# Optimization experiments

Measured on AMD Instinct MI355X. Metric: run time of the kernel, lower is better.

Reference implementation:

```python
import jax, jax.numpy as jnp
import numpy as np

VOCAB = 50000
D = 128      # word_embedding_size
H = 64       # attention_hidden_dim


def _doc_embed(words, emb_table, w_self, b_self):
    """words: (..., W) int -> (..., D) via tanh self-attention pooling over words."""
    we = emb_table[words]                                # (..., W, D)
    scores = jnp.tanh(we @ w_self + b_self)              # (..., W, 1)
    wgt = jax.nn.softmax(scores, axis=-2)                # softmax over word dim
    return jnp.sum(wgt * we, axis=-2)                    # (..., D)


def _attention(reviews_emb, query_emb, Wq, bq, w_red):
    """reviews_emb: (B,R,D), query_emb: (B,1,D) -> (B,D)."""
    B = query_emb.shape[0]
    pq = jnp.tanh(query_emb.reshape(B, D) @ Wq + bq)     # (B, D*H)
    pq = pq.reshape(B, D, H)
    s = jnp.einsum('brd,bdh->brh', reviews_emb, pq)      # (B,R,H)
    r = s @ w_red                                        # (B,R,1)
    w = jax.nn.softmax(r, axis=1)                        # softmax over reviews
    return jnp.sum(w * reviews_emb, axis=1)              # (B,D)


def setup_inputs() -> dict:
    key = jax.random.key(0)
    ks = jax.random.split(key, 9)
    B, R, W = 256, 20, 100
    user = jax.random.randint(ks[0], (B, R, W), 0, VOCAB)
    item = jax.random.randint(ks[1], (B, R, W), 0, VOCAB)
    query = jax.random.randint(ks[2], (B, W), 0, VOCAB)
    emb_table = jax.random.normal(ks[3], (VOCAB, D), dtype=jnp.float32) * 0.01
    w_self = jax.random.normal(ks[4], (D, 1), dtype=jnp.float32) * (1.0 / np.sqrt(D))
    b_self = jax.random.uniform(ks[5], (1,), dtype=jnp.float32, maxval=0.01)
    Wq = jax.random.normal(ks[6], (D, D * H), dtype=jnp.float32) * (1.0 / np.sqrt(D))
    bq = jax.random.uniform(ks[7], (D * H,), dtype=jnp.float32, maxval=0.01)
    w_red = jax.random.normal(ks[8], (H, 1), dtype=jnp.float32) * (1.0 / np.sqrt(H))
    pf = jnp.float32(0.5)  # personalized_factor
    return {"user_reviews_words": user, "item_reviews_words": item, "query": query,
            "emb_table": emb_table, "w_self": w_self, "b_self": b_self,
            "Wq": Wq, "bq": bq, "w_red": w_red, "pf": pf}


def reference(user_reviews_words, item_reviews_words, query,
              emb_table, w_self, b_self, Wq, bq, w_red, pf):
    # mode == 'test'
    user_emb = _doc_embed(user_reviews_words, emb_table, w_self, b_self)   # (B,R,D)
    item_emb = _doc_embed(item_reviews_words, emb_table, w_self, b_self)   # (B,R,D)
    q_emb = _doc_embed(query[:, None, :], emb_table, w_self, b_self)       # (B,1,D)
    user_entity = _attention(user_emb, q_emb, Wq, bq, w_red)               # (B,D)
    item_entity = _attention(item_emb, q_emb, Wq, bq, w_red)               # (B,D)
    personalized = user_entity + pf * q_emb[:, 0, :]
    return (personalized, item_entity)
```

## Files before the change

### kernel.cpp

```cpp
#include <hip/hip_runtime.h>
#include <math.h>

#define D 128
#define H 64
#define W 100
#define R 20
#define NB 256
#define NDOC_UI (NB * R)
#define NDOC    (2 * NDOC_UI + NB)
#define VOCAB 50000

__device__ __forceinline__ float fast_tanh(float x) {
    float u = __expf(2.0f * x);
    return 1.0f - 2.0f * __builtin_amdgcn_rcpf(1.0f + u);
}
__device__ __forceinline__ float fast_exp_tanh(float x) {
    return __expf(fast_tanh(x));
}

__device__ __forceinline__ unsigned short f2bf(float f) {
    unsigned int b = __float_as_uint(f);
    b += 0x7fffu + ((b >> 16) & 1u);
    return (unsigned short)(b >> 16);
}

__global__ __launch_bounds__(256) void vocab_prep_kernel(
    const float* __restrict__ emb, const float* __restrict__ w_self,
    const float* __restrict__ b_self,
    ushort* __restrict__ emb_bf, float* __restrict__ evocab)
{
    int tid = threadIdx.x, lane32 = tid & 31, grp = tid >> 5;
    int row = blockIdx.x * 8 + grp;
    float4 v   = ((const float4*)emb)[row * 32 + lane32];
    float4 ws4 = ((const float4*)w_self)[lane32];
    float p = v.x * ws4.x + v.y * ws4.y + v.z * ws4.z + v.w * ws4.w;
    p += __shfl_xor(p, 16, 64);
    p += __shfl_xor(p, 8, 64);
    p += __shfl_xor(p, 4, 64);
    p += __shfl_xor(p, 2, 64);
    p += __shfl_xor(p, 1, 64);
    float e = __expf(tanhf(p + b_self[0]));
    if (lane32 == 0) evocab[row] = e;
    ushort4 u;
    u.x = f2bf(v.x * e); u.y = f2bf(v.y * e);
    u.z = f2bf(v.z * e); u.w = f2bf(v.w * e);
    int q = lane32 >> 3;
    ushort4* dst = (ushort4*)(emb_bf + (size_t)q * VOCAB * 32);
    dst[row * 8 + (lane32 & 7)] = u;
}

__global__ __launch_bounds__(128) void doc_embed_bf16_kernel(
    const int* __restrict__ user_w, const int* __restrict__ item_w,
    const int* __restrict__ query_w,
    const ushort* __restrict__ emb_bf, const float* __restrict__ evocab,
    float* __restrict__ user_emb, float* __restrict__ item_emb,
    float* __restrict__ q_emb)
{
    int tid    = threadIdx.x;
    int lane32 = tid & 31;
    int grp    = tid >> 5;
    unsigned B    = blockIdx.x;
    unsigned quar = (B & 7) >> 1;
    unsigned sub  = (B >> 3) * 2 + (B & 1);
    int doc = (int)sub * 4 + grp;

    const int* wp; float* outp;
    if (doc < NDOC_UI)        { wp = user_w + doc * W;               outp = user_emb + doc * D; }
    else if (doc < 2*NDOC_UI) { int t = doc - NDOC_UI;   wp = item_w  + t * W; outp = item_emb + t * D; }
    else                      { int t = doc - 2*NDOC_UI; wp = query_w + t * W; outp = q_emb    + t * D; }

    int wreg[4];
    #pragma unroll
    for (int k = 0; k < 4; ++k) {
        int idx = k * 32 + lane32;
        wreg[k] = wp[idx > W - 1 ? W - 1 : idx];
    }

    float ep = 0.f;
    #pragma unroll
    for (int k = 0; k < 4; ++k) {
        float e = evocab[wreg[k]];
        if (k < 3 || lane32 < 4) ep += e;
    }
    ep += __shfl_xor(ep, 16, 64);
    ep += __shfl_xor(ep, 8, 64);
    ep += __shfl_xor(ep, 4, 64);
    ep += __shfl_xor(ep, 2, 64);
    ep += __shfl_xor(ep, 1, 64);
    float inv = 1.f / ep;

    int permbase = (tid & 32) << 2;
    int wsub     = lane32 >> 2;
    int sext     = lane32 & 3;

    float acc[8];
    #pragma unroll
    for (int j = 0; j < 8; ++j) acc[j] = 0.f;

    const uint4* eq4 = (const uint4*)(emb_bf + (size_t)quar * VOCAB * 32);

    #pragma unroll
    for (int c = 0; c < 2; ++c) {
        const int n  = (c == 0) ? 7 : 6;
        const int s0 = (c == 0) ? 0 : 7;
        int wid[7]; uint4 v[7];
        for (int j = 0; j < n; ++j) {
            int s = s0 + j;
            wid[j] = __builtin_amdgcn_ds_bpermute(
                permbase | ((((8 * s) & 31) + wsub) << 2), wreg[s >> 2]);
        }
        for (int j = 0; j < n; ++j)
            v[j] = eq4[(size_t)(unsigned)wid[j] * 4 + sext];
        for (int j = 0; j < n; ++j) {
            if (s0 + j == 12 && wsub >= 4) break;
            uint4 x = v[j];
            acc[0] += __uint_as_float(x.x << 16);
            acc[1] += __uint_as_float(x.x & 0xffff0000u);
            acc[2] += __uint_as_float(x.y << 16);
            acc[3] += __uint_as_float(x.y & 0xffff0000u);
            acc[4] += __uint_as_float(x.z << 16);
            acc[5] += __uint_as_float(x.z & 0xffff0000u);
            acc[6] += __uint_as_float(x.w << 16);
            acc[7] += __uint_as_float(x.w & 0xffff0000u);
        }
    }

    #pragma unroll
    for (int j = 0; j < 8; ++j) {
        acc[j] += __shfl_xor(acc[j], 4, 64);
        acc[j] += __shfl_xor(acc[j], 8, 64);
        acc[j] += __shfl_xor(acc[j], 16, 64);
    }

    if (wsub == 0) {
        float* o = outp + quar * 32 + sext * 8;
        *(float4*)o       = make_float4(acc[0]*inv, acc[1]*inv, acc[2]*inv, acc[3]*inv);
        *(float4*)(o + 4) = make_float4(acc[4]*inv, acc[5]*inv, acc[6]*inv, acc[7]*inv);
    }
}

__global__ __launch_bounds__(256, 7) void doc_embed_fp32_kernel(
    const int* __restrict__ user_w, const int* __restrict__ item_w,
    const int* __restrict__ query_w,
    const float* __restrict__ emb, const float* __restrict__ w_self,
    const float* __restrict__ b_self,
    float* __restrict__ user_emb, float* __restrict__ item_emb,
    float* __restrict__ q_emb)
{
    int tid    = threadIdx.x;
    int lane32 = tid & 31;
    int grp    = tid >> 5;
    int doc    = blockIdx.x * 8 + grp;

    const int* wp; float* outp;
    if (doc < NDOC_UI)        { wp = user_w + doc * W;               outp = user_emb + doc * D; }
    else if (doc < 2*NDOC_UI) { int t = doc - NDOC_UI;   wp = item_w  + t * W; outp = item_emb + t * D; }
    else                      { int t = doc - 2*NDOC_UI; wp = query_w + t * W; outp = q_emb    + t * D; }

    int wreg[4];
    #pragma unroll
    for (int k = 0; k < 4; ++k) {
        int idx = k * 32 + lane32;
        wreg[k] = wp[idx > W - 1 ? W - 1 : idx];
    }

    float4 ws4 = ((const float4*)w_self)[lane32];
    float  bs  = b_self[0];
    const float4* emb4 = (const float4*)emb;
    int permbase = (tid & 32) * 4;

    float4 acc  = make_float4(0.f, 0.f, 0.f, 0.f);
    float  esum = 0.f;

    #pragma unroll
    for (int c = 0; c < 10; ++c) {
        int word[10];
        #pragma unroll
        for (int j = 0; j < 10; ++j) {
            int w = c * 10 + j;
            word[j] = __builtin_amdgcn_ds_bpermute(permbase | ((w & 31) * 4),
                                                   wreg[w >> 5]);
        }
        float4 v[10];
        #pragma unroll
        for (int j = 0; j < 10; ++j)
            v[j] = emb4[(size_t)word[j] * 32 + lane32];

        #pragma unroll
        for (int j = 0; j < 10; ++j) {
            float p = v[j].x * ws4.x + v[j].y * ws4.y + v[j].z * ws4.z + v[j].w * ws4.w;
            p += __shfl_xor(p, 16, 64);
            p += __shfl_xor(p, 8, 64);
            p += __shfl_xor(p, 4, 64);
            p += __shfl_xor(p, 2, 64);
            p += __shfl_xor(p, 1, 64);
            float e = fast_exp_tanh(p + bs);
            esum += e;
            acc.x += e * v[j].x;
            acc.y += e * v[j].y;
            acc.z += e * v[j].z;
            acc.w += e * v[j].w;
        }
    }

    float inv = 1.0f / esum;
    acc.x *= inv; acc.y *= inv; acc.z *= inv; acc.w *= inv;
    ((float4*)outp)[lane32] = acc;
}

__global__ __launch_bounds__(256) void pv_kernel(
    const float* __restrict__ q_emb, const float* __restrict__ Wq,
    const float* __restrict__ bq, const float* __restrict__ w_red,
    float* __restrict__ pv)
{
    __shared__ __align__(16) float Wb[128 * 68];

    int dd  = blockIdx.x;
    int m0g = blockIdx.y * 128;
    int tid = threadIdx.x;

    {
        int rrow = tid >> 4;
        int f4   = tid & 15;
        #pragma unroll
        for (int pass = 0; pass < 8; ++pass) {
            int k = pass * 16 + rrow;
            float4 vw = ((const float4*)Wq)[k * 2048 + dd * 16 + f4];
            *(float4*)&Wb[k * 68 + f4 * 4] = vw;
        }
    }
    __syncthreads();

    int nthr = tid & 15;
    int mthr = tid >> 4;
    int n0 = nthr * 4;
    const float4* q4 = (const float4*)q_emb;
    int mbase = (m0g + mthr * 8) * 32;

    float acc[8][4];
    #pragma unroll
    for (int i = 0; i < 8; ++i)
        #pragma unroll
        for (int j = 0; j < 4; ++j) acc[i][j] = 0.f;

    float4 qa[8], qb[8];
    #pragma unroll
    for (int i = 0; i < 8; ++i) qa[i] = q4[mbase + i * 32];

    for (int k4 = 0; k4 < 32; ++k4) {
        if (k4 < 31) {
            #pragma unroll
            for (int i = 0; i < 8; ++i) qb[i] = q4[mbase + i * 32 + k4 + 1];
        }
        #pragma unroll
        for (int kk = 0; kk < 4; ++kk) {
            float4 wv = *(const float4*)&Wb[(k4 * 4 + kk) * 68 + n0];
            #pragma unroll
            for (int i = 0; i < 8; ++i) {
                float a = (kk == 0) ? qa[i].x : (kk == 1) ? qa[i].y
                        : (kk == 2) ? qa[i].z : qa[i].w;
                acc[i][0] += a * wv.x;
                acc[i][1] += a * wv.y;
                acc[i][2] += a * wv.z;
                acc[i][3] += a * wv.w;
            }
        }
        #pragma unroll
        for (int i = 0; i < 8; ++i) qa[i] = qb[i];
    }

    float4 bqv = ((const float4*)bq)[dd * 16 + nthr];
    float4 wrv = ((const float4*)w_red)[nthr];

    #pragma unroll
    for (int i = 0; i < 8; ++i) {
        float s = fast_tanh(acc[i][0] + bqv.x) * wrv.x
                + fast_tanh(acc[i][1] + bqv.y) * wrv.y
                + fast_tanh(acc[i][2] + bqv.z) * wrv.z
                + fast_tanh(acc[i][3] + bqv.w) * wrv.w;
        s += __shfl_xor(s, 1, 64);
        s += __shfl_xor(s, 2, 64);
        s += __shfl_xor(s, 4, 64);
        s += __shfl_xor(s, 8, 64);
        if (nthr == 0) pv[(m0g + mthr * 8 + i) * 128 + dd] = s;
    }
}

__global__ __launch_bounds__(256) void attn_kernel(
    const float* __restrict__ user_emb, const float* __restrict__ item_emb,
    const float* __restrict__ q_emb, const float* __restrict__ pv,
    const float* __restrict__ pf, float* __restrict__ out)
{
    __shared__ float rev[R * 129];
    __shared__ float pvl[D];
    __shared__ float sc[R];

    int b   = blockIdx.x;
    int set = blockIdx.y;
    const float* revg = (set == 0 ? user_emb : item_emb) + b * R * D;
    int tid = threadIdx.x;

    for (int idx = tid; idx < R * D; idx += 256)
        rev[(idx >> 7) * 129 + (idx & 127)] = revg[idx];
    if (tid < D) pvl[tid] = pv[b * D + tid];
    __syncthreads();

    if (tid < R) {
        float s = 0.f;
        const float* row = &rev[tid * 129];
        #pragma unroll 16
        for (int k = 0; k < D; ++k) s += row[k] * pvl[k];
        sc[tid] = s;
    }
    __syncthreads();

    float m = -1e30f;
    for (int r = 0; r < R; ++r) m = fmaxf(m, sc[r]);
    float sum = 0.f;
    for (int r = 0; r < R; ++r) sum += __expf(sc[r] - m);
    float inv = 1.f / sum;

    if (tid < D) {
        float acc = 0.f;
        for (int r = 0; r < R; ++r)
            acc += __expf(sc[r] - m) * inv * rev[r * 129 + tid];
        if (set == 0) {
            acc += pf[0] * q_emb[b * D + tid];
            out[b * D + tid] = acc;
        } else {
            out[NB * D + b * D + tid] = acc;
        }
    }
}

extern "C" void kernel_launch(void* const* d_in, const int* in_sizes, int n_in,
                              void* d_out, int out_size, void* d_ws, size_t ws_size,
                              hipStream_t stream) {
    const int*   user_w  = (const int*)d_in[0];
    const int*   item_w  = (const int*)d_in[1];
    const int*   query_w = (const int*)d_in[2];
    const float* emb     = (const float*)d_in[3];
    const float* w_self  = (const float*)d_in[4];
    const float* b_self  = (const float*)d_in[5];
    const float* Wq      = (const float*)d_in[6];
    const float* bq      = (const float*)d_in[7];
    const float* w_red   = (const float*)d_in[8];
    const float* pf      = (const float*)d_in[9];

    float* ws       = (float*)d_ws;
    float* user_emb = ws;
    float* item_emb = user_emb + NDOC_UI * D;
    float* q_emb    = item_emb + NDOC_UI * D;
    float* pv       = q_emb    + NB * D;
    float* evocab   = pv       + NB * D;
    ushort* emb_bf  = (ushort*)(evocab + VOCAB);
    float* out      = (float*)d_out;

    const size_t need_fast =
        (size_t)(2 * NDOC_UI * D + 2 * NB * D + VOCAB) * sizeof(float)
        + (size_t)VOCAB * D * sizeof(ushort);

    if (ws_size >= need_fast) {
        vocab_prep_kernel<<<VOCAB / 8, 256, 0, stream>>>(
            emb, w_self, b_self, emb_bf, evocab);
        doc_embed_bf16_kernel<<<NDOC, 128, 0, stream>>>(
            user_w, item_w, query_w, emb_bf, evocab, user_emb, item_emb, q_emb);
    } else {
        doc_embed_fp32_kernel<<<NDOC / 8, 256, 0, stream>>>(
            user_w, item_w, query_w, emb, w_self, b_self, user_emb, item_emb, q_emb);
    }
    pv_kernel<<<dim3(128, 2), 256, 0, stream>>>(q_emb, Wq, bq, w_red, pv);
    attn_kernel<<<dim3(NB, 2), 256, 0, stream>>>(user_emb, item_emb, q_emb, pv, pf, out);
}
```

Baseline: 146.3 us.

## Fuse all four stages into one persistent kernel with grid barriers

Replaces the vocab-prep, bf16 doc-embed, pv and attention launches with a single persistent kernel of 256 blocks of 512 threads. The stages are separated by atomic-counter grid barriers, and the counters are reset with a memset before each launch. This removes launch gaps and tail effects between kernels. In exchange, the doc-embed phase runs with only 256 resident blocks instead of thousands, which may lower memory-level parallelism for the gather. Correctness also depends on every block being co-resident.

```diff
diff --git a/kernel.cpp b/kernel.cpp
--- a/kernel.cpp
+++ b/kernel.cpp
@@ -9,6 +9,8 @@
 #define NDOC_UI (NB * R)
 #define NDOC    (2 * NDOC_UI + NB)
 #define VOCAB 50000
+#define GRID 256
+#define TPB  512
 
 __device__ __forceinline__ float fast_tanh(float x) {
     float u = __expf(2.0f * x);
@@ -24,118 +26,254 @@
     return (unsigned short)(b >> 16);
 }
 
-__global__ __launch_bounds__(256) void vocab_prep_kernel(
+__device__ __forceinline__ void grid_barrier(unsigned* cnt) {
+    __syncthreads();
+    if (threadIdx.x == 0) {
+        __hip_atomic_fetch_add(cnt, 1u, __ATOMIC_ACQ_REL, __HIP_MEMORY_SCOPE_AGENT);
+        while (__hip_atomic_load(cnt, __ATOMIC_ACQUIRE, __HIP_MEMORY_SCOPE_AGENT) < GRID)
+            __builtin_amdgcn_s_sleep(8);
+    }
+    __syncthreads();
+}
+
+__global__ __launch_bounds__(TPB, 4) void fused_kernel(
+    const int* __restrict__ user_w, const int* __restrict__ item_w,
+    const int* __restrict__ query_w,
     const float* __restrict__ emb, const float* __restrict__ w_self,
     const float* __restrict__ b_self,
-    ushort* __restrict__ emb_bf, float* __restrict__ evocab)
+    const float* __restrict__ Wq, const float* __restrict__ bq,
+    const float* __restrict__ w_red, const float* __restrict__ pf,
+    float* __restrict__ user_emb, float* __restrict__ item_emb,
+    float* __restrict__ q_emb, float* __restrict__ pv,
+    float* __restrict__ evocab, ushort* __restrict__ emb_bf,
+    unsigned* __restrict__ sync_cnt,
+    float* __restrict__ out)
 {
-    int tid = threadIdx.x, lane32 = tid & 31, grp = tid >> 5;
-    int row = blockIdx.x * 8 + grp;
-    float4 v   = ((const float4*)emb)[row * 32 + lane32];
-    float4 ws4 = ((const float4*)w_self)[lane32];
-    float p = v.x * ws4.x + v.y * ws4.y + v.z * ws4.z + v.w * ws4.w;
-    p += __shfl_xor(p, 16, 64);
-    p += __shfl_xor(p, 8, 64);
-    p += __shfl_xor(p, 4, 64);
-    p += __shfl_xor(p, 2, 64);
-    p += __shfl_xor(p, 1, 64);
-    float e = __expf(tanhf(p + b_self[0]));
-    if (lane32 == 0) evocab[row] = e;
-    ushort4 u;
-    u.x = f2bf(v.x * e); u.y = f2bf(v.y * e);
-    u.z = f2bf(v.z * e); u.w = f2bf(v.w * e);
-    int q = lane32 >> 3;
-    ushort4* dst = (ushort4*)(emb_bf + (size_t)q * VOCAB * 32);
-    dst[row * 8 + (lane32 & 7)] = u;
-}
-
-__global__ __launch_bounds__(128) void doc_embed_bf16_kernel(
-    const int* __restrict__ user_w, const int* __restrict__ item_w,
-    const int* __restrict__ query_w,
-    const ushort* __restrict__ emb_bf, const float* __restrict__ evocab,
-    float* __restrict__ user_emb, float* __restrict__ item_emb,
-    float* __restrict__ q_emb)
-{
-    int tid    = threadIdx.x;
-    int lane32 = tid & 31;
-    int grp    = tid >> 5;
-    unsigned B    = blockIdx.x;
-    unsigned quar = (B & 7) >> 1;
-    unsigned sub  = (B >> 3) * 2 + (B & 1);
-    int doc = (int)sub * 4 + grp;
-
-    const int* wp; float* outp;
-    if (doc < NDOC_UI)        { wp = user_w + doc * W;               outp = user_emb + doc * D; }
-    else if (doc < 2*NDOC_UI) { int t = doc - NDOC_UI;   wp = item_w  + t * W; outp = item_emb + t * D; }
-    else                      { int t = doc - 2*NDOC_UI; wp = query_w + t * W; outp = q_emb    + t * D; }
-
-    int wreg[4];
-    #pragma unroll
-    for (int k = 0; k < 4; ++k) {
-        int idx = k * 32 + lane32;
-        wreg[k] = wp[idx > W - 1 ? W - 1 : idx];
-    }
-
-    float ep = 0.f;
-    #pragma unroll
-    for (int k = 0; k < 4; ++k) {
-        float e = evocab[wreg[k]];
-        if (k < 3 || lane32 < 4) ep += e;
-    }
-    ep += __shfl_xor(ep, 16, 64);
-    ep += __shfl_xor(ep, 8, 64);
-    ep += __shfl_xor(ep, 4, 64);
-    ep += __shfl_xor(ep, 2, 64);
-    ep += __shfl_xor(ep, 1, 64);
-    float inv = 1.f / ep;
-
-    int permbase = (tid & 32) << 2;
-    int wsub     = lane32 >> 2;
-    int sext     = lane32 & 3;
-
-    float acc[8];
-    #pragma unroll
-    for (int j = 0; j < 8; ++j) acc[j] = 0.f;
-
-    const uint4* eq4 = (const uint4*)(emb_bf + (size_t)quar * VOCAB * 32);
-
-    #pragma unroll
-    for (int c = 0; c < 2; ++c) {
-        const int n  = (c == 0) ? 7 : 6;
-        const int s0 = (c == 0) ? 0 : 7;
-        int wid[7]; uint4 v[7];
-        for (int j = 0; j < n; ++j) {
-            int s = s0 + j;
-            wid[j] = __builtin_amdgcn_ds_bpermute(
-                permbase | ((((8 * s) & 31) + wsub) << 2), wreg[s >> 2]);
-        }
-        for (int j = 0; j < n; ++j)
-            v[j] = eq4[(size_t)(unsigned)wid[j] * 4 + sext];
-        for (int j = 0; j < n; ++j) {
-            if (s0 + j == 12 && wsub >= 4) break;
-            uint4 x = v[j];
-            acc[0] += __uint_as_float(x.x << 16);
-            acc[1] += __uint_as_float(x.x & 0xffff0000u);
-            acc[2] += __uint_as_float(x.y << 16);
-            acc[3] += __uint_as_float(x.y & 0xffff0000u);
-            acc[4] += __uint_as_float(x.z << 16);
-            acc[5] += __uint_as_float(x.z & 0xffff0000u);
-            acc[6] += __uint_as_float(x.w << 16);
-            acc[7] += __uint_as_float(x.w & 0xffff0000u);
-        }
-    }
-
-    #pragma unroll
-    for (int j = 0; j < 8; ++j) {
-        acc[j] += __shfl_xor(acc[j], 4, 64);
-        acc[j] += __shfl_xor(acc[j], 8, 64);
-        acc[j] += __shfl_xor(acc[j], 16, 64);
-    }
-
-    if (wsub == 0) {
-        float* o = outp + quar * 32 + sext * 8;
-        *(float4*)o       = make_float4(acc[0]*inv, acc[1]*inv, acc[2]*inv, acc[3]*inv);
-        *(float4*)(o + 4) = make_float4(acc[4]*inv, acc[5]*inv, acc[6]*inv, acc[7]*inv);
+    __shared__ __align__(16) float smem[128 * 68];
+    const int tid    = threadIdx.x;
+    const int bx     = blockIdx.x;
+    const int lane32 = tid & 31;
+
+    {
+        const int grp16 = tid >> 5;
+        float4 ws4 = ((const float4*)w_self)[lane32];
+        float  bs  = b_self[0];
+        for (int row = bx * 16 + grp16; row < VOCAB; row += GRID * 16) {
+            float4 v = ((const float4*)emb)[row * 32 + lane32];
+            float p = v.x * ws4.x + v.y * ws4.y + v.z * ws4.z + v.w * ws4.w;
+            p += __shfl_xor(p, 16, 64);
+            p += __shfl_xor(p, 8, 64);
+            p += __shfl_xor(p, 4, 64);
+            p += __shfl_xor(p, 2, 64);
+            p += __shfl_xor(p, 1, 64);
+            float e = __expf(tanhf(p + bs));
+            if (lane32 == 0) evocab[row] = e;
+            ushort4 u;
+            u.x = f2bf(v.x * e); u.y = f2bf(v.y * e);
+            u.z = f2bf(v.z * e); u.w = f2bf(v.w * e);
+            int q = lane32 >> 3;
+            ushort4* dst = (ushort4*)(emb_bf + (size_t)q * VOCAB * 32);
+            dst[row * 8 + (lane32 & 7)] = u;
+        }
+    }
+    grid_barrier(&sync_cnt[0]);
+
+    {
+        const int quar = (bx & 7) >> 1;
+        const int rb   = ((bx >> 3) << 1) | (bx & 1);
+        const int g    = tid >> 5;
+        const int permbase = (tid & 32) << 2;
+        const int wsub = lane32 >> 2;
+        const int sext = lane32 & 3;
+        const uint4* eq4 = (const uint4*)(emb_bf + (size_t)quar * VOCAB * 32);
+
+        for (int it = 0; it < 11; ++it) {
+            int local = it * 16 + g;
+            if (local >= 164) break;
+            int doc = rb * 164 + local;
+
+            const int* wp; float* outp;
+            if (doc < NDOC_UI)        { wp = user_w + doc * W;               outp = user_emb + doc * D; }
+            else if (doc < 2*NDOC_UI) { int t2 = doc - NDOC_UI;   wp = item_w  + t2 * W; outp = item_emb + t2 * D; }
+            else                      { int t2 = doc - 2*NDOC_UI; wp = query_w + t2 * W; outp = q_emb    + t2 * D; }
+
+            int wreg[4];
+            #pragma unroll
+            for (int k = 0; k < 4; ++k) {
+                int idx = k * 32 + lane32;
+                wreg[k] = wp[idx > W - 1 ? W - 1 : idx];
+            }
+
+            float ep = 0.f;
+            #pragma unroll
+            for (int k = 0; k < 4; ++k) {
+                float e = evocab[wreg[k]];
+                if (k < 3 || lane32 < 4) ep += e;
+            }
+            ep += __shfl_xor(ep, 16, 64);
+            ep += __shfl_xor(ep, 8, 64);
+            ep += __shfl_xor(ep, 4, 64);
+            ep += __shfl_xor(ep, 2, 64);
+            ep += __shfl_xor(ep, 1, 64);
+            float inv = 1.f / ep;
+
+            float acc[8];
+            #pragma unroll
+            for (int j = 0; j < 8; ++j) acc[j] = 0.f;
+
+            #pragma unroll
+            for (int c = 0; c < 2; ++c) {
+                const int n  = (c == 0) ? 7 : 6;
+                const int s0 = (c == 0) ? 0 : 7;
+                int wid[7]; uint4 v[7];
+                for (int j = 0; j < n; ++j) {
+                    int s = s0 + j;
+                    wid[j] = __builtin_amdgcn_ds_bpermute(
+                        permbase | ((((8 * s) & 31) + wsub) << 2), wreg[s >> 2]);
+                }
+                for (int j = 0; j < n; ++j)
+                    v[j] = eq4[(size_t)(unsigned)wid[j] * 4 + sext];
+                for (int j = 0; j < n; ++j) {
+                    if (s0 + j == 12 && wsub >= 4) break;
+                    uint4 x = v[j];
+                    acc[0] += __uint_as_float(x.x << 16);
+                    acc[1] += __uint_as_float(x.x & 0xffff0000u);
+                    acc[2] += __uint_as_float(x.y << 16);
+                    acc[3] += __uint_as_float(x.y & 0xffff0000u);
+                    acc[4] += __uint_as_float(x.z << 16);
+                    acc[5] += __uint_as_float(x.z & 0xffff0000u);
+                    acc[6] += __uint_as_float(x.w << 16);
+                    acc[7] += __uint_as_float(x.w & 0xffff0000u);
+                }
+            }
+
+            #pragma unroll
+            for (int j = 0; j < 8; ++j) {
+                acc[j] += __shfl_xor(acc[j], 4, 64);
+                acc[j] += __shfl_xor(acc[j], 8, 64);
+                acc[j] += __shfl_xor(acc[j], 16, 64);
+            }
+
+            if (wsub == 0) {
+                float* o = outp + quar * 32 + sext * 8;
+                *(float4*)o       = make_float4(acc[0]*inv, acc[1]*inv, acc[2]*inv, acc[3]*inv);
+                *(float4*)(o + 4) = make_float4(acc[4]*inv, acc[5]*inv, acc[6]*inv, acc[7]*inv);
+            }
+        }
+    }
+    grid_barrier(&sync_cnt[1]);
+
+    {
+        const int dd  = bx >> 1;
+        const int m0g = (bx & 1) * 128;
+        {
+            int rrow = tid >> 4;
+            int f4   = tid & 15;
+            #pragma unroll
+            for (int pass = 0; pass < 4; ++pass) {
+                int k = pass * 32 + rrow;
+                float4 vw = ((const float4*)Wq)[k * 2048 + dd * 16 + f4];
+                *(float4*)&smem[k * 68 + f4 * 4] = vw;
+            }
+        }
+        __syncthreads();
+
+        int nthr = tid & 15;
+        int mthr = tid >> 4;
+        int n0 = nthr * 4;
+        const float4* q4 = (const float4*)q_emb;
+        int mbase = m0g + mthr * 4;
+
+        float acc[4][4];
+        #pragma unroll
+        for (int i = 0; i < 4; ++i)
+            #pragma unroll
+            for (int j = 0; j < 4; ++j) acc[i][j] = 0.f;
+
+        float4 qa[4], qb[4];
+        #pragma unroll
+        for (int i = 0; i < 4; ++i) qa[i] = q4[(mbase + i) * 32];
+
+        for (int k4 = 0; k4 < 32; ++k4) {
+            if (k4 < 31) {
+                #pragma unroll
+                for (int i = 0; i < 4; ++i) qb[i] = q4[(mbase + i) * 32 + k4 + 1];
+            }
+            #pragma unroll
+            for (int kk = 0; kk < 4; ++kk) {
+                float4 wv = *(const float4*)&smem[(k4 * 4 + kk) * 68 + n0];
+                #pragma unroll
+                for (int i = 0; i < 4; ++i) {
+                    float a = (kk == 0) ? qa[i].x : (kk == 1) ? qa[i].y
+                            : (kk == 2) ? qa[i].z : qa[i].w;
+                    acc[i][0] += a * wv.x;
+                    acc[i][1] += a * wv.y;
+                    acc[i][2] += a * wv.z;
+                    acc[i][3] += a * wv.w;
+                }
+            }
+            #pragma unroll
+            for (int i = 0; i < 4; ++i) qa[i] = qb[i];
+        }
+
+        float4 bqv = ((const float4*)bq)[dd * 16 + nthr];
+        float4 wrv = ((const float4*)w_red)[nthr];
+
+        #pragma unroll
+        for (int i = 0; i < 4; ++i) {
+            float s = fast_tanh(acc[i][0] + bqv.x) * wrv.x
+                    + fast_tanh(acc[i][1] + bqv.y) * wrv.y
+                    + fast_tanh(acc[i][2] + bqv.z) * wrv.z
+                    + fast_tanh(acc[i][3] + bqv.w) * wrv.w;
+            s += __shfl_xor(s, 1, 64);
+            s += __shfl_xor(s, 2, 64);
+            s += __shfl_xor(s, 4, 64);
+            s += __shfl_xor(s, 8, 64);
+            if (nthr == 0) pv[(mbase + i) * 128 + dd] = s;
+        }
+    }
+    grid_barrier(&sync_cnt[2]);
+
+    {
+        const int b   = bx;
+        const int set = tid >> 8;
+        const int t   = tid & 255;
+        const float* revg = (set == 0 ? user_emb : item_emb) + b * R * D;
+        float* srev = smem + set * (R * 129);
+        float* pvl  = smem + 2 * (R * 129);
+        float* ssc  = smem + 2 * (R * 129) + D + set * 32;
+
+        for (int idx = t; idx < R * D; idx += 256)
+            srev[(idx >> 7) * 129 + (idx & 127)] = revg[idx];
+        if (tid < D) pvl[tid] = pv[b * D + tid];
+        __syncthreads();
+
+        if (t < R) {
+            float s = 0.f;
+            const float* row = &srev[t * 129];
+            #pragma unroll 16
+            for (int k = 0; k < D; ++k) s += row[k] * pvl[k];
+            ssc[t] = s;
+        }
+        __syncthreads();
+
+        float m = -1e30f;
+        for (int r = 0; r < R; ++r) m = fmaxf(m, ssc[r]);
+        float sum = 0.f;
+        for (int r = 0; r < R; ++r) sum += __expf(ssc[r] - m);
+        float inv = 1.f / sum;
+
+        if (t < D) {
+            float acc2 = 0.f;
+            for (int r = 0; r < R; ++r)
+                acc2 += __expf(ssc[r] - m) * inv * srev[r * 129 + t];
+            if (set == 0) {
+                acc2 += pf[0] * q_emb[b * D + t];
+                out[b * D + t] = acc2;
+            } else {
+                out[NB * D + b * D + t] = acc2;
+            }
+        }
     }
 }
 
@@ -354,21 +492,23 @@
     float* pv       = q_emb    + NB * D;
     float* evocab   = pv       + NB * D;
     ushort* emb_bf  = (ushort*)(evocab + VOCAB);
+    unsigned* sync_cnt = (unsigned*)(emb_bf + (size_t)VOCAB * D);
     float* out      = (float*)d_out;
 
     const size_t need_fast =
         (size_t)(2 * NDOC_UI * D + 2 * NB * D + VOCAB) * sizeof(float)
-        + (size_t)VOCAB * D * sizeof(ushort);
+        + (size_t)VOCAB * D * sizeof(ushort)
+        + 3 * sizeof(unsigned);
 
     if (ws_size >= need_fast) {
-        vocab_prep_kernel<<<VOCAB / 8, 256, 0, stream>>>(
-            emb, w_self, b_self, emb_bf, evocab);
-        doc_embed_bf16_kernel<<<NDOC, 128, 0, stream>>>(
-            user_w, item_w, query_w, emb_bf, evocab, user_emb, item_emb, q_emb);
+        hipMemsetAsync(sync_cnt, 0, 3 * sizeof(unsigned), stream);
+        fused_kernel<<<GRID, TPB, 0, stream>>>(
+            user_w, item_w, query_w, emb, w_self, b_self, Wq, bq, w_red, pf,
+            user_emb, item_emb, q_emb, pv, evocab, emb_bf, sync_cnt, out);
     } else {
         doc_embed_fp32_kernel<<<NDOC / 8, 256, 0, stream>>>(
             user_w, item_w, query_w, emb, w_self, b_self, user_emb, item_emb, q_emb);
-    }
-    pv_kernel<<<dim3(128, 2), 256, 0, stream>>>(q_emb, Wq, bq, w_red, pv);
-    attn_kernel<<<dim3(NB, 2), 256, 0, stream>>>(user_emb, item_emb, q_emb, pv, pf, out);
-}
+        pv_kernel<<<dim3(128, 2), 256, 0, stream>>>(q_emb, Wq, bq, w_red, pv);
+        attn_kernel<<<dim3(NB, 2), 256, 0, stream>>>(user_emb, item_emb, q_emb, pv, pf, out);
+    }
+}
```

Result: slower. 214.3 us (+46.4%).
